# Kernel optimization log

Hardware: AMD Instinct MI355X
Metric: run time of the kernel (lower is better)

Reference implementation:

```python
import jax, jax.numpy as jnp
import numpy as np

N = 100000   # nodes
E = 1600000  # edges
F_IN = 256   # nfeat
H = 64       # hidden_sizes
C = 40       # nclass


def gcn_norm(edge_index, edge_weight, num_nodes):
    # Add self-loops with weight 1 (PyG gcn_norm default fill_value=1.0)
    loop = jnp.arange(num_nodes)
    row = jnp.concatenate([edge_index[0], loop])
    col = jnp.concatenate([edge_index[1], loop])
    w = jnp.concatenate([edge_weight, jnp.ones((num_nodes,), edge_weight.dtype)])
    # Symmetric normalization: D^-1/2 A D^-1/2 (degree computed at target, per PyG)
    deg = jax.ops.segment_sum(w, col, num_segments=num_nodes)
    deg_inv_sqrt = jnp.where(deg > 0, jax.lax.rsqrt(deg), 0.0)
    norm = deg_inv_sqrt[row] * w * deg_inv_sqrt[col]
    return row, col, norm


def gcn_conv(x, W, b, row, col, norm, num_nodes):
    # Linear transform first (shrinks feature dim before irregular traffic)
    x = x @ W                                    # [N, out]
    msgs = norm[:, None] * x[row]                # gather + scale: [E+N, out]
    out = jax.ops.segment_sum(msgs, col, num_segments=num_nodes)  # scatter-add
    return out + b


def setup_inputs() -> dict:
    key = jax.random.key(0)
    k = jax.random.split(key, 7)
    x = jax.random.normal(k[0], (N, F_IN), dtype=jnp.float32)
    edge_index = jax.random.randint(k[1], (2, E), 0, N, dtype=jnp.int64)
    edge_attr = jax.random.uniform(k[2], (E,), dtype=jnp.float32)
    W1 = jax.random.normal(k[3], (F_IN, H), dtype=jnp.float32) * (1.0 / np.sqrt(F_IN))
    b1 = jnp.zeros((H,), jnp.float32)
    W2 = jax.random.normal(k[4], (H, C), dtype=jnp.float32) * (1.0 / np.sqrt(H))
    b2 = jnp.zeros((C,), jnp.float32)
    return {"x": x, "edge_index": edge_index, "edge_attr": edge_attr,
            "W1": W1, "b1": b1, "W2": W2, "b2": b2}


def reference(x, edge_index, edge_attr, W1, b1, W2, b2):
    row, col, norm = gcn_norm(edge_index, edge_attr, N)
    h = jax.nn.relu(gcn_conv(x, W1, b1, row, col, norm, N))
    # F.dropout with training=False is identity (eval mode)
    final = gcn_conv(h, W2, b2, row, col, norm, N)
    return final, jax.nn.log_softmax(final, axis=1)
```

## Files before the change

### kernel.cpp

```cpp
#include <hip/hip_runtime.h>
#include <hip/hip_bf16.h>
#include <math.h>

#define NN 100000
#define EE 1600000
#define FIN 256
#define HID 64
#define NC 40
#define NB 196
#define BCAP 10240
#define CHUNK 2048
#define NBKB ((EE + CHUNK - 1) / CHUNK)

typedef unsigned long long ull;
typedef __attribute__((ext_vector_type(2))) unsigned long long ullx2;
typedef __attribute__((ext_vector_type(8))) short short8;
typedef __attribute__((ext_vector_type(4))) float f32x4;

__device__ __forceinline__ unsigned short f2bf_rne(float f) {
    unsigned u = __float_as_uint(f);
    u += 0x7FFFu + ((u >> 16) & 1u);
    return (unsigned short)(u >> 16);
}
__device__ __forceinline__ float bf2f(unsigned short b) {
    return __uint_as_float((unsigned)b << 16);
}

__device__ __forceinline__ void edge_acc(ull q, const unsigned* __restrict__ tbl,
                                         int fl, float& a0, float& a1) {
    unsigned src = (unsigned)q & 0x1FFFFu;
    unsigned u = tbl[(src << 5) | fl];
    float w = __int_as_float((int)(q >> 32));
    a0 += w * __uint_as_float(u << 16);
    a1 += w * __uint_as_float(u & 0xFFFF0000u);
}

__global__ __launch_bounds__(256) void bucket_kernel(const int* __restrict__ row,
                                                     const int* __restrict__ col,
                                                     const float* __restrict__ w,
                                                     int* __restrict__ bucket_cnt,
                                                     int2* __restrict__ staging) {
    __shared__ int2 spay[CHUNK];
    __shared__ int2 sorted[CHUNK];
    __shared__ unsigned char sb[CHUNK];
    __shared__ unsigned char sbk[CHUNK];
    __shared__ int lcnt[NB], lofs[NB], lstart[NB];
    __shared__ int sscan[256];
    const int tid = threadIdx.x;
    const int e0 = blockIdx.x * CHUNK;
    const int nE = min(CHUNK, EE - e0);
    for (int i = tid; i < nE; i += 256) {
        int e = e0 + i;
        int c = col[e];
        sb[i] = (unsigned char)(c >> 9);
        spay[i] = make_int2(((c & 511) << 17) | row[e], __float_as_int(w[e]));
    }
    for (int i = tid; i < NB; i += 256) lcnt[i] = 0;
    __syncthreads();
    for (int i = tid; i < nE; i += 256) atomicAdd(&lcnt[sb[i]], 1);
    __syncthreads();
    int v = (tid < NB) ? lcnt[tid] : 0;
    sscan[tid] = v;
    __syncthreads();
    for (int off = 1; off < 256; off <<= 1) {
        int u = (tid >= off) ? sscan[tid - off] : 0;
        __syncthreads();
        sscan[tid] += u;
        __syncthreads();
    }
    if (tid < NB) {
        lofs[tid] = sscan[tid] - v;
        lstart[tid] = v ? atomicAdd(&bucket_cnt[tid], v) : 0;
        lcnt[tid] = 0;
    }
    __syncthreads();
    for (int i = tid; i < nE; i += 256) {
        int b = sb[i];
        int p = lofs[b] + atomicAdd(&lcnt[b], 1);
        sorted[p] = spay[i];
        sbk[p] = (unsigned char)b;
    }
    __syncthreads();
    for (int p = tid; p < nE; p += 256) {
        int b = sbk[p];
        int slot = lstart[b] + (p - lofs[b]);
        if (slot < BCAP) staging[(size_t)b * BCAP + slot] = sorted[p];
    }
}

__global__ __launch_bounds__(512) void build_count_kernel(const int2* __restrict__ staging,
                                                          const int* __restrict__ bucket_cnt,
                                                          int* __restrict__ basev,
                                                          int* __restrict__ endv,
                                                          float* __restrict__ dis,
                                                          int* __restrict__ ptot) {
    __shared__ int dcnt[512];
    __shared__ float dsum[512];
    __shared__ int sscan[512];
    const int t = threadIdx.x;
    const int b = blockIdx.x;
    const int nE = min(bucket_cnt[b], BCAP);
    const int2* st = staging + (size_t)b * BCAP;
    dcnt[t] = 0; dsum[t] = 0.f;
    __syncthreads();
    for (int i = t; i < nE; i += 512) {
        int2 p = st[i];
        int d = p.x >> 17;
        atomicAdd(&dcnt[d], 1);
        atomicAdd(&dsum[d], __int_as_float(p.y));
    }
    __syncthreads();
    int c = dcnt[t];
    int pdeg = (c + 7) & ~7;
    sscan[t] = pdeg;
    __syncthreads();
    for (int off = 1; off < 512; off <<= 1) {
        int u = (t >= off) ? sscan[t - off] : 0;
        __syncthreads();
        sscan[t] += u;
        __syncthreads();
    }
    int gd = b * 512 + t;
    if (gd < NN) {
        basev[gd] = sscan[t] - pdeg;
        endv[gd] = c;
        dis[gd] = rsqrtf(dsum[t] + 1.0f);
    }
    if (t == 511) ptot[b] = sscan[511];
}

__global__ __launch_bounds__(256) void bscan_w1cvt_kernel(const int* __restrict__ ptot,
                                                          int* __restrict__ bucket_base,
                                                          const float* __restrict__ W1,
                                                          unsigned short* __restrict__ w1hi,
                                                          unsigned short* __restrict__ w1lo) {
    if (blockIdx.x == 0) {
        __shared__ int sd[256];
        int t = threadIdx.x;
        int v = (t < NB) ? ptot[t] : 0;
        sd[t] = v;
        __syncthreads();
        for (int off = 1; off < 256; off <<= 1) {
            int u = (t >= off) ? sd[t - off] : 0;
            __syncthreads();
            sd[t] += u;
            __syncthreads();
        }
        if (t < NB) bucket_base[t] = sd[t] - v;
    } else {
        int b = blockIdx.x - 1;
        for (int i = threadIdx.x; i < 4096; i += 256) {
            int e = b * 4096 + i;
            int c = e >> 8, k = e & 255;
            float v = W1[(size_t)k * HID + c];
            unsigned short h = f2bf_rne(v);
            w1hi[e] = h;
            w1lo[e] = f2bf_rne(v - bf2f(h));
        }
    }
}

__global__ __launch_bounds__(512) void build_place_kernel(const int2* __restrict__ staging,
                                                          const int* __restrict__ bucket_cnt,
                                                          const int* __restrict__ bucket_base,
                                                          int* __restrict__ basev,
                                                          int* __restrict__ endv,
                                                          const float* __restrict__ dis,
                                                          int2* __restrict__ eme) {
    __shared__ int dcur[512];
    __shared__ float sdis[512];
    const int t = threadIdx.x;
    const int b = blockIdx.x;
    const int nE = min(bucket_cnt[b], BCAP);
    const int2* st = staging + (size_t)b * BCAP;
    const int gd = b * 512 + t;
    int gb = 0, c = 0, pdeg = 0;
    if (gd < NN) {
        gb = bucket_base[b] + basev[gd];
        c = endv[gd];
        pdeg = (c + 7) & ~7;
        basev[gd] = gb;
        endv[gd] = gb + c;
        sdis[t] = dis[gd];
    } else {
        sdis[t] = 0.f;
    }
    dcur[t] = gb;
    __syncthreads();
    for (int i = t; i < nE; i += 512) {
        int2 p = st[i];
        int d = p.x >> 17;
        int src = p.x & 0x1FFFF;
        int pos = atomicAdd(&dcur[d], 1);
        float wn = __int_as_float(p.y) * dis[src] * sdis[d];
        eme[pos] = make_int2(src, __float_as_int(wn));
    }
    for (int i = c; i < pdeg; i++) eme[gb + i] = make_int2(0, 0);
}

__global__ __launch_bounds__(256, 4) void gemm1_mfma_kernel(const float* __restrict__ x,
                                                            const unsigned short* __restrict__ w1hi,
                                                            const unsigned short* __restrict__ w1lo,
                                                            __hip_bfloat16* __restrict__ xw) {
    const int tid = threadIdx.x;
    const int wid = tid >> 6;
    const int l   = tid & 63;
    const int r   = l & 15;
    const int kg  = l >> 4;
    const int rb0 = blockIdx.x * 64 + wid * 16;

    f32x4 acc[4];
#pragma unroll
    for (int j = 0; j < 4; j++) acc[j] = (f32x4){0.f, 0.f, 0.f, 0.f};

    int row0 = rb0 + r;
    int row0c = row0 < NN ? row0 : NN - 1;
    const float* ap = x + (size_t)row0c * FIN + kg * 8;
    const unsigned short* bp = w1hi + (size_t)r * FIN + kg * 8;
    const unsigned short* lp = w1lo + (size_t)r * FIN + kg * 8;

    short8 bhi[2][4], blo[2][4];
#pragma unroll
    for (int ct = 0; ct < 4; ct++) {
        bhi[0][ct] = *(const short8*)(bp + (size_t)ct * 16 * FIN);
        blo[0][ct] = *(const short8*)(lp + (size_t)ct * 16 * FIN);
    }
#pragma unroll
    for (int ks = 0; ks < 8; ks++) {
        const int cur = ks & 1, nxt = cur ^ 1;
        if (ks < 7) {
#pragma unroll
            for (int ct = 0; ct < 4; ct++) {
                bhi[nxt][ct] = *(const short8*)(bp + (size_t)ct * 16 * FIN + (ks + 1) * 32);
                blo[nxt][ct] = *(const short8*)(lp + (size_t)ct * 16 * FIN + (ks + 1) * 32);
            }
        }
        float4 afa = *(const float4*)(ap + ks * 32);
        float4 afb = *(const float4*)(ap + ks * 32 + 4);
        float av[8] = {afa.x, afa.y, afa.z, afa.w, afb.x, afb.y, afb.z, afb.w};
        short8 ahi, alo;
#pragma unroll
        for (int j = 0; j < 8; j++) {
            unsigned short h = f2bf_rne(av[j]);
            ahi[j] = (short)h;
            alo[j] = (short)f2bf_rne(av[j] - bf2f(h));
        }
#pragma unroll
        for (int ct = 0; ct < 4; ct++) {
            acc[ct] = __builtin_amdgcn_mfma_f32_16x16x32_bf16(ahi, bhi[cur][ct], acc[ct], 0, 0, 0);
            acc[ct] = __builtin_amdgcn_mfma_f32_16x16x32_bf16(ahi, blo[cur][ct], acc[ct], 0, 0, 0);
            acc[ct] = __builtin_amdgcn_mfma_f32_16x16x32_bf16(alo, bhi[cur][ct], acc[ct], 0, 0, 0);
        }
    }
#pragma unroll
    for (int i = 0; i < 4; i++) {
        int grow = rb0 + kg * 4 + i;
        if (grow < NN) {
            unsigned short* dst = (unsigned short*)xw + (size_t)grow * HID + r;
#pragma unroll
            for (int ct = 0; ct < 4; ct++)
                dst[ct * 16] = f2bf_rne(acc[ct][i]);
        }
    }
}

__global__ __launch_bounds__(256) void gather1_kernel(const int* __restrict__ basev,
                                                      const int* __restrict__ endv,
                                                      const ull* __restrict__ eme,
                                                      const unsigned* __restrict__ xw32,
                                                      const float* __restrict__ dis,
                                                      const float* __restrict__ b,
                                                      float* __restrict__ h) {
    int n = blockIdx.x * 4 + (threadIdx.x >> 6);
    if (n >= NN) return;
    int lane = threadIdx.x & 63;
    int half = lane >> 5;
    int fl = lane & 31;
    int s = basev[n], t = endv[n];
    int pdeg = (t - s + 7) & ~7;
    float acc0 = 0.f, acc1 = 0.f;
    int nb16 = pdeg >> 4;
    for (int bi = 0; bi < nb16; bi++) {
        const ull* pp = eme + s + bi * 16 + 8 * half;
        ullx2 qa = *(const ullx2*)(pp);
        ullx2 qb = *(const ullx2*)(pp + 2);
        ullx2 qc = *(const ullx2*)(pp + 4);
        ullx2 qd = *(const ullx2*)(pp + 6);
        edge_acc(qa[0], xw32, fl, acc0, acc1);
        edge_acc(qa[1], xw32, fl, acc0, acc1);
        edge_acc(qb[0], xw32, fl, acc0, acc1);
        edge_acc(qb[1], xw32, fl, acc0, acc1);
        edge_acc(qc[0], xw32, fl, acc0, acc1);
        edge_acc(qc[1], xw32, fl, acc0, acc1);
        edge_acc(qd[0], xw32, fl, acc0, acc1);
        edge_acc(qd[1], xw32, fl, acc0, acc1);
    }
    if (pdeg & 8) {
        const ull* pp = eme + s + nb16 * 16 + 4 * half;
        ullx2 qa = *(const ullx2*)(pp);
        ullx2 qb = *(const ullx2*)(pp + 2);
        edge_acc(qa[0], xw32, fl, acc0, acc1);
        edge_acc(qa[1], xw32, fl, acc0, acc1);
        edge_acc(qb[0], xw32, fl, acc0, acc1);
        edge_acc(qb[1], xw32, fl, acc0, acc1);
    }
    acc0 += __shfl_xor(acc0, 32);
    acc1 += __shfl_xor(acc1, 32);
    float d = dis[n];
    unsigned un = xw32[((unsigned)n << 5) | fl];
    float2 bv = *(const float2*)(b + 2 * fl);
    float v0 = acc0 + d * d * __uint_as_float(un << 16) + bv.x;
    float v1 = acc1 + d * d * __uint_as_float(un & 0xFFFF0000u) + bv.y;
    if (lane < 32) {
        *(float2*)(h + (size_t)n * HID + 2 * fl) = make_float2(fmaxf(v0, 0.f), fmaxf(v1, 0.f));
    }
}

__global__ __launch_bounds__(256) void gemm2_kernel(const float* __restrict__ h,
                                                    const float* __restrict__ W,
                                                    __hip_bfloat16* __restrict__ hw) {
    __shared__ float hs[64][65];
    __shared__ float Ws[HID * NC];
    const int tid = threadIdx.x;
    const int base = blockIdx.x * 64;
    for (int v = tid; v < 1024; v += 256) {
        int r = v >> 4, q = v & 15;
        int gr = base + r;
        float4 hv = make_float4(0.f, 0.f, 0.f, 0.f);
        if (gr < NN) hv = *(const float4*)(h + (size_t)gr * HID + q * 4);
        hs[r][q * 4 + 0] = hv.x; hs[r][q * 4 + 1] = hv.y;
        hs[r][q * 4 + 2] = hv.z; hs[r][q * 4 + 3] = hv.w;
    }
    for (int v = tid; v < HID * NC; v += 256) Ws[v] = W[v];
    __syncthreads();
    const int tx = tid & 7;
    const int ty = tid >> 3;
    float acc[2][5] = {};
#pragma unroll 8
    for (int k = 0; k < HID; k++) {
        float h0 = hs[ty * 2 + 0][k];
        float h1 = hs[ty * 2 + 1][k];
        const float* wr = &Ws[k * NC + tx * 5];
        float w0 = wr[0], w1 = wr[1], w2 = wr[2], w3 = wr[3], w4 = wr[4];
        acc[0][0] += h0 * w0; acc[0][1] += h0 * w1; acc[0][2] += h0 * w2;
        acc[0][3] += h0 * w3; acc[0][4] += h0 * w4;
        acc[1][0] += h1 * w0; acc[1][1] += h1 * w1; acc[1][2] += h1 * w2;
        acc[1][3] += h1 * w3; acc[1][4] += h1 * w4;
    }
#pragma unroll
    for (int i = 0; i < 2; i++) {
        int gr = base + ty * 2 + i;
        if (gr < NN) {
#pragma unroll
            for (int c = 0; c < 5; c++)
                hw[(size_t)gr * 64 + tx * 5 + c] = __float2bfloat16(acc[i][c]);
        }
    }
}

__global__ __launch_bounds__(256) void gather2_kernel(const int* __restrict__ basev,
                                                      const int* __restrict__ endv,
                                                      const ull* __restrict__ eme,
                                                      const unsigned* __restrict__ hw32,
                                                      const float* __restrict__ dis,
                                                      const float* __restrict__ b,
                                                      float* __restrict__ out) {
    int n = blockIdx.x * 4 + (threadIdx.x >> 6);
    if (n >= NN) return;
    int lane = threadIdx.x & 63;
    int half = lane >> 5;
    int fl = lane & 31;
    bool act = fl < 20;
    int s = basev[n], t = endv[n];
    int pdeg = (t - s + 7) & ~7;
    float acc0 = 0.f, acc1 = 0.f;
    int nb16 = pdeg >> 4;
    for (int bi = 0; bi < nb16; bi++) {
        const ull* pp = eme + s + bi * 16 + 8 * half;
        ullx2 qa = *(const ullx2*)(pp);
        ullx2 qb = *(const ullx2*)(pp + 2);
        ullx2 qc = *(const ullx2*)(pp + 4);
        ullx2 qd = *(const ullx2*)(pp + 6);
        edge_acc(qa[0], hw32, fl, acc0, acc1);
        edge_acc(qa[1], hw32, fl, acc0, acc1);
        edge_acc(qb[0], hw32, fl, acc0, acc1);
        edge_acc(qb[1], hw32, fl, acc0, acc1);
        edge_acc(qc[0], hw32, fl, acc0, acc1);
        edge_acc(qc[1], hw32, fl, acc0, acc1);
        edge_acc(qd[0], hw32, fl, acc0, acc1);
        edge_acc(qd[1], hw32, fl, acc0, acc1);
    }
    if (pdeg & 8) {
        const ull* pp = eme + s + nb16 * 16 + 4 * half;
        ullx2 qa = *(const ullx2*)(pp);
        ullx2 qb = *(const ullx2*)(pp + 2);
        edge_acc(qa[0], hw32, fl, acc0, acc1);
        edge_acc(qa[1], hw32, fl, acc0, acc1);
        edge_acc(qb[0], hw32, fl, acc0, acc1);
        edge_acc(qb[1], hw32, fl, acc0, acc1);
    }
    acc0 += __shfl_xor(acc0, 32);
    acc1 += __shfl_xor(acc1, 32);
    float v0 = 0.f, v1 = 0.f, m = -INFINITY;
    if (act) {
        float d = dis[n];
        unsigned un = hw32[((unsigned)n << 5) | fl];
        float2 bv = *(const float2*)(b + 2 * fl);
        v0 = acc0 + d * d * __uint_as_float(un << 16) + bv.x;
        v1 = acc1 + d * d * __uint_as_float(un & 0xFFFF0000u) + bv.y;
        m = fmaxf(v0, v1);
    }
#pragma unroll
    for (int off = 16; off; off >>= 1) m = fmaxf(m, __shfl_xor(m, off));
    float e0 = act ? expf(v0 - m) : 0.f;
    float e1 = act ? expf(v1 - m) : 0.f;
    float sum = e0 + e1;
#pragma unroll
    for (int off = 16; off; off >>= 1) sum += __shfl_xor(sum, off);
    float lse = m + logf(sum);
    if (act && lane < 32) {
        size_t idx = (size_t)n * NC + 2 * fl;
        *(float2*)(out + idx) = make_float2(v0, v1);
        *(float2*)(out + (size_t)NN * NC + idx) = make_float2(v0 - lse, v1 - lse);
    }
}

extern "C" void kernel_launch(void* const* d_in, const int* in_sizes, int n_in,
                              void* d_out, int out_size, void* d_ws, size_t ws_size,
                              hipStream_t stream) {
    const float* x    = (const float*)d_in[0];
    const int*   eidx = (const int*)d_in[1];
    const float* ew   = (const float*)d_in[2];
    const float* W1   = (const float*)d_in[3];
    const float* b1   = (const float*)d_in[4];
    const float* W2   = (const float*)d_in[5];
    const float* b2   = (const float*)d_in[6];
    float* out = (float*)d_out;

    const int* row = eidx;
    const int* col = eidx + EE;

    char* ws = (char*)d_ws;
    int*   bucket_cnt  = (int*)ws;               ws += 256 * 4;
    int*   bucket_base = (int*)ws;               ws += 256 * 4;
    int*   ptot        = (int*)ws;               ws += 256 * 4;
    float* dis    = (float*)ws;                  ws += NN * 4;
    int*   basev  = (int*)ws;                    ws += NN * 4;
    int*   endv   = (int*)ws;                    ws += NN * 4;
    int2*  eme    = (int2*)ws;                   ws += ((size_t)EE + 8 * NN) * 8;
    __hip_bfloat16* xw = (__hip_bfloat16*)ws;    ws += (size_t)NN * HID * 2;
    char* unionp = ws;                           ws += (size_t)NN * HID * 4;
    int2*  staging = (int2*)unionp;
    float* h       = (float*)unionp;
    __hip_bfloat16* hw2 = (__hip_bfloat16*)ws;   ws += (size_t)NN * 64 * 2;
    unsigned short* w1hi = (unsigned short*)ws;  ws += (size_t)HID * FIN * 2;
    unsigned short* w1lo = (unsigned short*)ws;  ws += (size_t)HID * FIN * 2;

    hipMemsetAsync(bucket_cnt, 0, 256 * 4, stream);

    bucket_kernel<<<NBKB, 256, 0, stream>>>(row, col, ew, bucket_cnt, staging);
    build_count_kernel<<<NB, 512, 0, stream>>>(staging, bucket_cnt,
                                               basev, endv, dis, ptot);
    bscan_w1cvt_kernel<<<5, 256, 0, stream>>>(ptot, bucket_base, W1, w1hi, w1lo);
    build_place_kernel<<<NB, 512, 0, stream>>>(staging, bucket_cnt, bucket_base,
                                               basev, endv, dis, eme);
    gemm1_mfma_kernel<<<(NN + 63) / 64, 256, 0, stream>>>(x, w1hi, w1lo, xw);
    gather1_kernel<<<(NN + 3) / 4, 256, 0, stream>>>(basev, endv, (const ull*)eme,
                                                     (const unsigned*)xw, dis, b1, h);
    gemm2_kernel<<<(NN + 63) / 64, 256, 0, stream>>>(h, W2, hw2);
    gather2_kernel<<<(NN + 3) / 4, 256, 0, stream>>>(basev, endv, (const ull*)eme,
                                                     (const unsigned*)hw2, dis, b2, out);
}
```

Measured before the change: 389.1 us.

## Stage W1 hi/lo tiles in LDS and double block size in gemm1

The first GEMM now stages the bf16 hi/lo split of W1 into shared memory in two phases of four k-slices. Previously each wave loaded its B fragments straight from global memory with register double-buffering. Blocks grow from 256 to 512 threads covering 128 rows, so each staged tile is shared by eight waves. This aims to cut redundant global/L2 traffic for W1, at the cost of extra barriers, 32KB of LDS per block and no overlap between the weight loads and the MFMAs.

```diff
diff --git a/kernel.cpp b/kernel.cpp
--- a/kernel.cpp
+++ b/kernel.cpp
@@ -198,16 +198,18 @@
     for (int i = c; i < pdeg; i++) eme[gb + i] = make_int2(0, 0);
 }
 
-__global__ __launch_bounds__(256, 4) void gemm1_mfma_kernel(const float* __restrict__ x,
+__global__ __launch_bounds__(512, 4) void gemm1_mfma_kernel(const float* __restrict__ x,
                                                             const unsigned short* __restrict__ w1hi,
                                                             const unsigned short* __restrict__ w1lo,
                                                             __hip_bfloat16* __restrict__ xw) {
+    __shared__ unsigned short shi[4096 * 2];
+    __shared__ unsigned short slo[4096 * 2];
     const int tid = threadIdx.x;
     const int wid = tid >> 6;
     const int l   = tid & 63;
     const int r   = l & 15;
     const int kg  = l >> 4;
-    const int rb0 = blockIdx.x * 64 + wid * 16;
+    const int rb0 = blockIdx.x * 128 + wid * 16;
 
     f32x4 acc[4];
 #pragma unroll
@@ -216,41 +218,41 @@
     int row0 = rb0 + r;
     int row0c = row0 < NN ? row0 : NN - 1;
     const float* ap = x + (size_t)row0c * FIN + kg * 8;
-    const unsigned short* bp = w1hi + (size_t)r * FIN + kg * 8;
-    const unsigned short* lp = w1lo + (size_t)r * FIN + kg * 8;
-
-    short8 bhi[2][4], blo[2][4];
-#pragma unroll
-    for (int ct = 0; ct < 4; ct++) {
-        bhi[0][ct] = *(const short8*)(bp + (size_t)ct * 16 * FIN);
-        blo[0][ct] = *(const short8*)(lp + (size_t)ct * 16 * FIN);
-    }
-#pragma unroll
-    for (int ks = 0; ks < 8; ks++) {
-        const int cur = ks & 1, nxt = cur ^ 1;
-        if (ks < 7) {
+
+#pragma unroll
+    for (int ph = 0; ph < 2; ph++) {
+        for (int c2 = tid; c2 < 1024; c2 += 512) {
+            int ckg = c2 & 3, ccol = (c2 >> 2) & 63, cksl = c2 >> 8;
+            size_t src = (size_t)ccol * FIN + (ph * 4 + cksl) * 32 + ckg * 8;
+            int dst = ((cksl * 64 + ccol) * 32 + ckg * 8);
+            *(short8*)(shi + dst) = *(const short8*)(w1hi + src);
+            *(short8*)(slo + dst) = *(const short8*)(w1lo + src);
+        }
+        __syncthreads();
+#pragma unroll
+        for (int ksl = 0; ksl < 4; ksl++) {
+            const int ks = ph * 4 + ksl;
+            float4 afa = *(const float4*)(ap + ks * 32);
+            float4 afb = *(const float4*)(ap + ks * 32 + 4);
+            float av[8] = {afa.x, afa.y, afa.z, afa.w, afb.x, afb.y, afb.z, afb.w};
+            short8 ahi, alo;
+#pragma unroll
+            for (int j = 0; j < 8; j++) {
+                unsigned short hh = f2bf_rne(av[j]);
+                ahi[j] = (short)hh;
+                alo[j] = (short)f2bf_rne(av[j] - bf2f(hh));
+            }
 #pragma unroll
             for (int ct = 0; ct < 4; ct++) {
-                bhi[nxt][ct] = *(const short8*)(bp + (size_t)ct * 16 * FIN + (ks + 1) * 32);
-                blo[nxt][ct] = *(const short8*)(lp + (size_t)ct * 16 * FIN + (ks + 1) * 32);
+                int bo = ((ksl * 64 + ct * 16 + r) * 32 + kg * 8);
+                short8 bh = *(const short8*)(shi + bo);
+                short8 bl = *(const short8*)(slo + bo);
+                acc[ct] = __builtin_amdgcn_mfma_f32_16x16x32_bf16(ahi, bh, acc[ct], 0, 0, 0);
+                acc[ct] = __builtin_amdgcn_mfma_f32_16x16x32_bf16(ahi, bl, acc[ct], 0, 0, 0);
+                acc[ct] = __builtin_amdgcn_mfma_f32_16x16x32_bf16(alo, bh, acc[ct], 0, 0, 0);
             }
         }
-        float4 afa = *(const float4*)(ap + ks * 32);
-        float4 afb = *(const float4*)(ap + ks * 32 + 4);
-        float av[8] = {afa.x, afa.y, afa.z, afa.w, afb.x, afb.y, afb.z, afb.w};
-        short8 ahi, alo;
-#pragma unroll
-        for (int j = 0; j < 8; j++) {
-            unsigned short h = f2bf_rne(av[j]);
-            ahi[j] = (short)h;
-            alo[j] = (short)f2bf_rne(av[j] - bf2f(h));
-        }
-#pragma unroll
-        for (int ct = 0; ct < 4; ct++) {
-            acc[ct] = __builtin_amdgcn_mfma_f32_16x16x32_bf16(ahi, bhi[cur][ct], acc[ct], 0, 0, 0);
-            acc[ct] = __builtin_amdgcn_mfma_f32_16x16x32_bf16(ahi, blo[cur][ct], acc[ct], 0, 0, 0);
-            acc[ct] = __builtin_amdgcn_mfma_f32_16x16x32_bf16(alo, bhi[cur][ct], acc[ct], 0, 0, 0);
-        }
+        __syncthreads();
     }
 #pragma unroll
     for (int i = 0; i < 4; i++) {
@@ -464,7 +466,7 @@
     bscan_w1cvt_kernel<<<5, 256, 0, stream>>>(ptot, bucket_base, W1, w1hi, w1lo);
     build_place_kernel<<<NB, 512, 0, stream>>>(staging, bucket_cnt, bucket_base,
                                                basev, endv, dis, eme);
-    gemm1_mfma_kernel<<<(NN + 63) / 64, 256, 0, stream>>>(x, w1hi, w1lo, xw);
+    gemm1_mfma_kernel<<<(NN + 127) / 128, 512, 0, stream>>>(x, w1hi, w1lo, xw);
     gather1_kernel<<<(NN + 3) / 4, 256, 0, stream>>>(basev, endv, (const ull*)eme,
                                                      (const unsigned*)xw, dis, b1, h);
     gemm2_kernel<<<(NN + 63) / 64, 256, 0, stream>>>(h, W2, hw2);
```

After: 357.5 us. -8.1%, faster.
